# Optimization experiments

Hardware: AMD Instinct MI355X
Metric: run time of the kernel (lower is better)

Reference implementation:

```python
import jax, jax.numpy as jnp
import numpy as np

OUTDIM, INPUTDIM, DEGREE = 64, 512, 8


def setup_inputs() -> dict:
    key = jax.random.key(0)
    k1, k2 = jax.random.split(key)
    x = jax.random.normal(k1, (16, 4096, INPUTDIM), dtype=jnp.float32)
    # torch.randn(outdim, inputdim, degree) / (sqrt(inputdim)*sqrt(degree))
    coeffs = jax.random.normal(k2, (OUTDIM, INPUTDIM, DEGREE), dtype=jnp.float32)
    coeffs = coeffs / (np.sqrt(INPUTDIM) * np.sqrt(DEGREE))
    bias = jnp.zeros((1, OUTDIM), dtype=jnp.float32)
    return {"x": x, "coeffs": coeffs, "bias": bias}


def _legendre_basis(xn, degree):
    # Iterative (memoized) Legendre recurrence; xn in [-1, 1], shape [N, I].
    Ps = [jnp.ones_like(xn)]
    if degree > 1:
        Ps.append(xn)
    for n in range(2, degree):
        Ps.append(((2.0 * n - 1.0) * xn * Ps[-1] - (n - 1.0) * Ps[-2]) / n)
    return jnp.stack(Ps, axis=-1)  # [N, I, D]


def reference(x, coeffs, bias):
    outdim, inputdim, degree = coeffs.shape
    outshape = x.shape[:-1] + (outdim,)
    x2 = x.reshape(-1, inputdim)                      # [N, I]
    xmin, xmax = x2.min(), x2.max()                   # global min-max normalize
    xn = 2.0 * (x2 - xmin) / (xmax - xmin) - 1.0
    P = _legendre_basis(xn, degree)                   # [N, I, D]
    y = jnp.einsum("nid,oid->no", P, coeffs)          # contract input & degree
    y = y + bias                                      # [N, O]
    return y.reshape(outshape)
```

## Files before the change

### kernel.cpp

```cpp
#include <hip/hip_runtime.h>
#include <math.h>


typedef __bf16 bf16x8 __attribute__((ext_vector_type(8)));
typedef float f32x4 __attribute__((ext_vector_type(4)));

__global__ __launch_bounds__(256) void k_minmax_partial(
    const float4* __restrict__ x4, int n4, float* __restrict__ pmn, float* __restrict__ pmx)
{
  float mn = 3.4e38f, mx = -3.4e38f;
  int stride = gridDim.x * 256;
  for (int i = blockIdx.x * 256 + threadIdx.x; i < n4; i += stride) {
    float4 v = x4[i];
    mn = fminf(mn, fminf(fminf(v.x, v.y), fminf(v.z, v.w)));
    mx = fmaxf(mx, fmaxf(fmaxf(v.x, v.y), fmaxf(v.z, v.w)));
  }
  #pragma unroll
  for (int off = 32; off > 0; off >>= 1) {
    mn = fminf(mn, __shfl_down(mn, off));
    mx = fmaxf(mx, __shfl_down(mx, off));
  }
  __shared__ float smn[4], smx[4];
  int w = threadIdx.x >> 6;
  if ((threadIdx.x & 63) == 0) { smn[w] = mn; smx[w] = mx; }
  __syncthreads();
  if (threadIdx.x == 0) {
    pmn[blockIdx.x] = fminf(fminf(smn[0], smn[1]), fminf(smn[2], smn[3]));
    pmx[blockIdx.x] = fmaxf(fmaxf(smx[0], smx[1]), fmaxf(smx[2], smx[3]));
  }
}

__global__ __launch_bounds__(256) void k_prep_final(
    const float* __restrict__ coeffs, bf16x8* __restrict__ Bws,
    const float* __restrict__ pmn, const float* __restrict__ pmx, int nb,
    float* __restrict__ so)
{
  if (blockIdx.x < 128) {
    int t = blockIdx.x * 256 + threadIdx.x;
    int lane = t & 63;
    int tile = t >> 6;
    int ct = tile & 3;
    int kt = tile >> 2;
    int i = kt * 4 + (lane >> 4);
    int o = ct * 16 + (lane & 15);
    const float4* cp = (const float4*)(coeffs + ((size_t)o * 512 + i) * 8);
    float4 c0 = cp[0], c1 = cp[1];
    bf16x8 v;
    v[0] = (__bf16)(c0.x);
    v[1] = (__bf16)(c0.y);
    v[2] = (__bf16)(c0.z * 1.5f);
    v[3] = (__bf16)(c0.w * 2.5f);
    v[4] = (__bf16)(c1.x * 4.375f);
    v[5] = (__bf16)(c1.y * 7.875f);
    v[6] = (__bf16)(c1.z * 14.4375f);
    v[7] = (__bf16)(c1.w * 26.8125f);
    Bws[(size_t)(kt * 4 + ct) * 64 + lane] = v;
  } else {
    float mn = 3.4e38f, mx = -3.4e38f;
    for (int i = threadIdx.x; i < nb; i += 256) {
      mn = fminf(mn, pmn[i]);
      mx = fmaxf(mx, pmx[i]);
    }
    #pragma unroll
    for (int off = 32; off > 0; off >>= 1) {
      mn = fminf(mn, __shfl_down(mn, off));
      mx = fmaxf(mx, __shfl_down(mx, off));
    }
    __shared__ float smn[4], smx[4];
    int w = threadIdx.x >> 6;
    if ((threadIdx.x & 63) == 0) { smn[w] = mn; smx[w] = mx; }
    __syncthreads();
    if (threadIdx.x == 0) {
      mn = fminf(fminf(smn[0], smn[1]), fminf(smn[2], smn[3]));
      mx = fmaxf(fmaxf(smx[0], smx[1]), fmaxf(smx[2], smx[3]));
      float r = mx - mn;
      so[0] = 2.0f / r;
      so[1] = -2.0f * mn / r - 1.0f;
    }
  }
}

#define LSTW 20
__global__ __launch_bounds__(256, 3) void k_main(
    const float* __restrict__ x, const bf16x8* __restrict__ Bws,
    const float* __restrict__ bias, const float* __restrict__ so,
    float* __restrict__ y)
{
  __shared__ char smem[49152];

  const float s = so[0], off = so[1];
  const int t    = threadIdx.x;
  const int lane = t & 63;
  const int w    = t >> 6;
  const int m    = lane & 15;
  const int quad = lane >> 4;
  const size_t blockRow = (size_t)blockIdx.x * 64;

  float* xsw = (float*)(smem + w * (2 * 64 * LSTW * 4));
  const float* xg = x + (blockRow + lane) * 512 + w * 128;

  int rb[4];
  #pragma unroll
  for (int f = 0; f < 4; ++f) rb[f] = (f * 16 + m) * LSTW + quad;

  const bf16x8* Bp = Bws + (size_t)w * 32 * 256 + lane;

  f32x4 acc[4][4];
  #pragma unroll
  for (int f = 0; f < 4; ++f)
    #pragma unroll
    for (int ct = 0; ct < 4; ++ct) acc[f][ct] = (f32x4){0.f, 0.f, 0.f, 0.f};

  const float C2 = 0.33333334f, C3 = 0.26666668f, C4 = 0.25714287f;
  const float C5 = 0.25396827f, C6 = 0.25252524f, C7 = 0.25174826f;

  float4 st[4];
  #pragma unroll
  for (int p = 0; p < 4; ++p) st[p] = *(const float4*)(xg + p * 4);
  #pragma unroll
  for (int p = 0; p < 4; ++p) *(float4*)&xsw[lane * LSTW + p * 4] = st[p];

  bf16x8 Bq[4][4];
  #pragma unroll
  for (int ct = 0; ct < 4; ++ct) {
    Bq[0][ct] = Bp[ct * 64];
    Bq[1][ct] = Bp[256 + ct * 64];
  }

  for (int c = 0; c < 8; ++c) {
    float* xr = xsw + (c & 1) * (64 * LSTW);

    if (c < 7) {
      const float* gp = xg + (c + 1) * 16;
      #pragma unroll
      for (int p = 0; p < 4; ++p) st[p] = *(const float4*)(gp + p * 4);
    }

    float xv[2][4];
    #pragma unroll
    for (int f = 0; f < 4; ++f) xv[0][f] = xr[rb[f]];

    #pragma unroll
    for (int ktl = 0; ktl < 4; ++ktl) {
      const int l = c * 4 + ktl;

      {
        const int kp = (l + 2) & 31;
        const bf16x8* bpk = Bp + (size_t)kp * 256;
        #pragma unroll
        for (int ct = 0; ct < 4; ++ct) Bq[(ktl + 2) & 3][ct] = bpk[ct * 64];
      }
      if (ktl < 3) {
        #pragma unroll
        for (int f = 0; f < 4; ++f)
          xv[(ktl + 1) & 1][f] = xr[rb[f] + (ktl + 1) * 4];
      }

      bf16x8 a[4];
      #pragma unroll
      for (int f = 0; f < 4; ++f) {
        float xn = fmaf(xv[ktl & 1][f], s, off);
        float s2 = fmaf(xn, xn, -C2);
        float s3 = (s2 - C3) * xn;
        float s4 = fmaf(xn, s3, -(C4 * s2));
        float s5 = fmaf(xn, s4, -(C5 * s3));
        float s6 = fmaf(xn, s5, -(C6 * s4));
        float s7 = fmaf(xn, s6, -(C7 * s5));
        bf16x8 av;
        av[0] = (__bf16)1.0f; av[1] = (__bf16)xn; av[2] = (__bf16)s2; av[3] = (__bf16)s3;
        av[4] = (__bf16)s4;   av[5] = (__bf16)s5; av[6] = (__bf16)s6; av[7] = (__bf16)s7;
        a[f] = av;
      }

      #pragma unroll
      for (int f = 0; f < 4; ++f)
        #pragma unroll
        for (int ct = 0; ct < 4; ++ct)
          acc[f][ct] = __builtin_amdgcn_mfma_f32_16x16x32_bf16(a[f], Bq[ktl & 3][ct], acc[f][ct], 0, 0, 0);
    }

    if (c < 7) {
      float* xw = xsw + ((c + 1) & 1) * (64 * LSTW);
      #pragma unroll
      for (int p = 0; p < 4; ++p) *(float4*)&xw[lane * LSTW + p * 4] = st[p];
    }
  }

  __syncthreads();
  f32x4* red = (f32x4*)smem;
  if (w > 0) {
    #pragma unroll
    for (int f = 0; f < 4; ++f)
      #pragma unroll
      for (int ct = 0; ct < 4; ++ct)
        red[(size_t)(w - 1) * 1024 + (f * 4 + ct) * 64 + lane] = acc[f][ct];
  }
  __syncthreads();
  if (w == 0) {
    #pragma unroll
    for (int f = 0; f < 4; ++f)
      #pragma unroll
      for (int ct = 0; ct < 4; ++ct) {
        f32x4 v = acc[f][ct];
        v += red[(f * 4 + ct) * 64 + lane];
        v += red[1024 + (f * 4 + ct) * 64 + lane];
        v += red[2048 + (f * 4 + ct) * 64 + lane];
        acc[f][ct] = v;
      }
    float bv0 = bias[m], bv1 = bias[16 + m], bv2 = bias[32 + m], bv3 = bias[48 + m];
    #pragma unroll
    for (int f = 0; f < 4; ++f) {
      float* yp = y + (blockRow + f * 16 + quad * 4) * 64 + m;
      #pragma unroll
      for (int r = 0; r < 4; ++r) {
        float* ypr = yp + r * 64;
        ypr[0]  = acc[f][0][r] + bv0;
        ypr[16] = acc[f][1][r] + bv1;
        ypr[32] = acc[f][2][r] + bv2;
        ypr[48] = acc[f][3][r] + bv3;
      }
    }
  }
}

__global__ __launch_bounds__(256) void k_main_simple(
    const float* __restrict__ x, const float* __restrict__ coeffs,
    const float* __restrict__ bias, const float* __restrict__ so, float* __restrict__ y)
{
  const float s = so[0], off = so[1];
  const int lane = threadIdx.x & 63;
  const int w    = threadIdx.x >> 6;
  const int m    = lane & 15;
  const int quad = lane >> 4;
  const int rowA = blockIdx.x * 64 + w * 16 + m;
  const float* xp = x + (size_t)rowA * 512 + quad;

  f32x4 acc0 = {0.f,0.f,0.f,0.f}, acc1 = acc0, acc2 = acc0, acc3 = acc0;
  const float c3a = 5.f/3.f, c3b = 2.f/3.f, c6a = 11.f/6.f, c6b = 5.f/6.f, c7a = 13.f/7.f, c7b = 6.f/7.f;

  for (int kt = 0; kt < 128; ++kt) {
    float xv = xp[kt * 4];
    int i = kt * 4 + quad;
    bf16x8 b[4];
    #pragma unroll
    for (int ct = 0; ct < 4; ++ct) {
      const float* cp = coeffs + ((size_t)(ct * 16 + m) * 512 + i) * 8;
      #pragma unroll
      for (int j = 0; j < 8; ++j) b[ct][j] = (__bf16)cp[j];
    }
    float xn = fmaf(xv, s, off);
    float p2 = fmaf(1.5f * xn, xn, -0.5f);
    float p3 = fmaf(c3a * xn, p2, -(c3b * xn));
    float p4 = fmaf(1.75f * xn, p3, -(0.75f * p2));
    float p5 = fmaf(1.8f * xn, p4, -(0.8f * p3));
    float p6 = fmaf(c6a * xn, p5, -(c6b * p4));
    float p7 = fmaf(c7a * xn, p6, -(c7b * p5));
    bf16x8 a;
    a[0] = (__bf16)1.0f; a[1] = (__bf16)xn; a[2] = (__bf16)p2; a[3] = (__bf16)p3;
    a[4] = (__bf16)p4;   a[5] = (__bf16)p5; a[6] = (__bf16)p6; a[7] = (__bf16)p7;
    acc0 = __builtin_amdgcn_mfma_f32_16x16x32_bf16(a, b[0], acc0, 0, 0, 0);
    acc1 = __builtin_amdgcn_mfma_f32_16x16x32_bf16(a, b[1], acc1, 0, 0, 0);
    acc2 = __builtin_amdgcn_mfma_f32_16x16x32_bf16(a, b[2], acc2, 0, 0, 0);
    acc3 = __builtin_amdgcn_mfma_f32_16x16x32_bf16(a, b[3], acc3, 0, 0, 0);
  }
  float b0v = bias[m], b1v = bias[16+m], b2v = bias[32+m], b3v = bias[48+m];
  float* yp = y + ((size_t)(blockIdx.x * 64 + w * 16 + quad * 4)) * 64 + m;
  #pragma unroll
  for (int r = 0; r < 4; ++r) {
    yp[r*64+ 0] = acc0[r] + b0v;
    yp[r*64+16] = acc1[r] + b1v;
    yp[r*64+32] = acc2[r] + b2v;
    yp[r*64+48] = acc3[r] + b3v;
  }
}

extern "C" void kernel_launch(void* const* d_in, const int* in_sizes, int n_in,
                              void* d_out, int out_size, void* d_ws, size_t ws_size,
                              hipStream_t stream)
{
  const float* x      = (const float*)d_in[0];
  const float* coeffs = (const float*)d_in[1];
  const float* bias   = (const float*)d_in[2];
  float* y = (float*)d_out;

  long nx = (long)in_sizes[0];
  int  N  = (int)(nx / 512);
  int  n4 = (int)(nx / 4);

  float*  so  = (float*)d_ws;
  float*  pmn = (float*)d_ws + 16;
  float*  pmx = pmn + 4096;
  bf16x8* Bws = (bf16x8*)((char*)d_ws + 65536);

  const int MMB = 2048;
  k_minmax_partial<<<MMB, 256, 0, stream>>>((const float4*)x, n4, pmn, pmx);

  bool pre = ws_size >= (size_t)(65536 + 4096 * 64 * 2 + 4096);
  k_prep_final<<<129, 256, 0, stream>>>(coeffs, Bws, pmn, pmx, MMB, so);
  if (pre) {
    k_main<<<N / 64, 256, 0, stream>>>(x, Bws, bias, so, y);
  } else {
    k_main_simple<<<N / 64, 256, 0, stream>>>(x, coeffs, bias, so, y);
  }
}
```

Baseline: 252.3 us.

## Split K across blocks with atomic accumulation and LDS-staged coefficients

```diff
diff --git a/kernel.cpp b/kernel.cpp
--- a/kernel.cpp
+++ b/kernel.cpp
@@ -33,10 +33,13 @@
 __global__ __launch_bounds__(256) void k_prep_final(
     const float* __restrict__ coeffs, bf16x8* __restrict__ Bws,
     const float* __restrict__ pmn, const float* __restrict__ pmx, int nb,
-    float* __restrict__ so)
-{
-  if (blockIdx.x < 128) {
-    int t = blockIdx.x * 256 + threadIdx.x;
+    float* __restrict__ so, float* __restrict__ y, const float* __restrict__ bias,
+    int doB)
+{
+  int b = blockIdx.x;
+  if (b < 128) {
+    if (!doB) return;
+    int t = b * 256 + threadIdx.x;
     int lane = t & 63;
     int tile = t >> 6;
     int ct = tile & 3;
@@ -55,7 +58,7 @@
     v[6] = (__bf16)(c1.z * 14.4375f);
     v[7] = (__bf16)(c1.w * 26.8125f);
     Bws[(size_t)(kt * 4 + ct) * 64 + lane] = v;
-  } else {
+  } else if (b == 128) {
     float mn = 3.4e38f, mx = -3.4e38f;
     for (int i = threadIdx.x; i < nb; i += 256) {
       mn = fminf(mn, pmn[i]);
@@ -77,16 +80,23 @@
       so[0] = 2.0f / r;
       so[1] = -2.0f * mn / r - 1.0f;
     }
-  }
-}
-
-#define LSTW 20
-__global__ __launch_bounds__(256, 3) void k_main(
+  } else {
+    int base = (b - 129) * 1024;
+    const float4* b4 = (const float4*)bias;
+    float4* y4 = (float4*)y;
+    #pragma unroll
+    for (int r = 0; r < 4; ++r) {
+      int j = base + r * 256 + threadIdx.x;
+      y4[j] = b4[j & 15];
+    }
+  }
+}
+
+__global__ __launch_bounds__(256, 4) void k_main(
     const float* __restrict__ x, const bf16x8* __restrict__ Bws,
-    const float* __restrict__ bias, const float* __restrict__ so,
-    float* __restrict__ y)
-{
-  __shared__ char smem[49152];
+    const float* __restrict__ so, float* __restrict__ y)
+{
+  __shared__ __align__(16) float4 smem[2048];
 
   const float s = so[0], off = so[1];
   const int t    = threadIdx.x;
@@ -94,72 +104,65 @@
   const int w    = t >> 6;
   const int m    = lane & 15;
   const int quad = lane >> 4;
-  const size_t blockRow = (size_t)blockIdx.x * 64;
-
-  float* xsw = (float*)(smem + w * (2 * 64 * LSTW * 4));
-  const float* xg = x + (blockRow + lane) * 512 + w * 128;
-
-  int rb[4];
-  #pragma unroll
-  for (int f = 0; f < 4; ++f) rb[f] = (f * 16 + m) * LSTW + quad;
-
-  const bf16x8* Bp = Bws + (size_t)w * 32 * 256 + lane;
-
-  f32x4 acc[4][4];
-  #pragma unroll
-  for (int f = 0; f < 4; ++f)
+  const int bx   = blockIdx.x;
+  const int qK   = bx & 3;
+  const size_t rowbase = ((size_t)(bx >> 2)) * 128 + (size_t)w * 32;
+  const int kb0 = qK * 32;
+
+  const float* xq0 = x + (rowbase +      m) * 512 + (size_t)kb0 * 4 + quad;
+  const float* xq1 = x + (rowbase + 16 + m) * 512 + (size_t)kb0 * 4 + quad;
+
+  const float4* bsrc = (const float4*)((const char*)Bws + (size_t)kb0 * 4096);
+
+  f32x4 acc[2][4];
+  #pragma unroll
+  for (int f = 0; f < 2; ++f)
     #pragma unroll
     for (int ct = 0; ct < 4; ++ct) acc[f][ct] = (f32x4){0.f, 0.f, 0.f, 0.f};
 
   const float C2 = 0.33333334f, C3 = 0.26666668f, C4 = 0.25714287f;
   const float C5 = 0.25396827f, C6 = 0.25252524f, C7 = 0.25174826f;
 
-  float4 st[4];
-  #pragma unroll
-  for (int p = 0; p < 4; ++p) st[p] = *(const float4*)(xg + p * 4);
-  #pragma unroll
-  for (int p = 0; p < 4; ++p) *(float4*)&xsw[lane * LSTW + p * 4] = st[p];
-
-  bf16x8 Bq[4][4];
-  #pragma unroll
-  for (int ct = 0; ct < 4; ++ct) {
-    Bq[0][ct] = Bp[ct * 64];
-    Bq[1][ct] = Bp[256 + ct * 64];
-  }
-
-  for (int c = 0; c < 8; ++c) {
-    float* xr = xsw + (c & 1) * (64 * LSTW);
-
-    if (c < 7) {
-      const float* gp = xg + (c + 1) * 16;
-      #pragma unroll
-      for (int p = 0; p < 4; ++p) st[p] = *(const float4*)(gp + p * 4);
-    }
-
-    float xv[2][4];
-    #pragma unroll
-    for (int f = 0; f < 4; ++f) xv[0][f] = xr[rb[f]];
-
-    #pragma unroll
-    for (int ktl = 0; ktl < 4; ++ktl) {
-      const int l = c * 4 + ktl;
-
+  float xr[4][2];
+  xr[0][0] = xq0[0];  xr[0][1] = xq1[0];
+  xr[1][0] = xq0[4];  xr[1][1] = xq1[4];
+
+  const bf16x8* bw = (const bf16x8*)smem;
+
+  for (int wi = 0; wi < 4; ++wi) {
+    __syncthreads();
+    {
+      const float4* g = bsrc + (size_t)wi * 2048;
+      float4 a0 = g[t], a1 = g[t + 256], a2 = g[t + 512], a3 = g[t + 768];
+      smem[t] = a0; smem[t + 256] = a1; smem[t + 512] = a2; smem[t + 768] = a3;
+      float4 b0 = g[t + 1024], b1 = g[t + 1280], b2 = g[t + 1536], b3 = g[t + 1792];
+      smem[t + 1024] = b0; smem[t + 1280] = b1; smem[t + 1536] = b2; smem[t + 1792] = b3;
+    }
+    __syncthreads();
+
+    bf16x8 Bq[2][4];
+    #pragma unroll
+    for (int ct = 0; ct < 4; ++ct) Bq[0][ct] = bw[ct * 64 + lane];
+
+    #pragma unroll
+    for (int kl = 0; kl < 8; ++kl) {
+      const int l = wi * 8 + kl;
+
+      if (kl < 7) {
+        #pragma unroll
+        for (int ct = 0; ct < 4; ++ct)
+          Bq[(kl + 1) & 1][ct] = bw[((kl + 1) * 4 + ct) * 64 + lane];
+      }
       {
-        const int kp = (l + 2) & 31;
-        const bf16x8* bpk = Bp + (size_t)kp * 256;
-        #pragma unroll
-        for (int ct = 0; ct < 4; ++ct) Bq[(ktl + 2) & 3][ct] = bpk[ct * 64];
+        const int lp = (l + 2 < 32) ? (l + 2) : 31;
+        xr[(kl + 2) & 3][0] = xq0[lp * 4];
+        xr[(kl + 2) & 3][1] = xq1[lp * 4];
       }
-      if (ktl < 3) {
-        #pragma unroll
-        for (int f = 0; f < 4; ++f)
-          xv[(ktl + 1) & 1][f] = xr[rb[f] + (ktl + 1) * 4];
-      }
-
-      bf16x8 a[4];
-      #pragma unroll
-      for (int f = 0; f < 4; ++f) {
-        float xn = fmaf(xv[ktl & 1][f], s, off);
+
+      bf16x8 a[2];
+      #pragma unroll
+      for (int f = 0; f < 2; ++f) {
+        float xn = fmaf(xr[kl & 3][f], s, off);
         float s2 = fmaf(xn, xn, -C2);
         float s3 = (s2 - C3) * xn;
         float s4 = fmaf(xn, s3, -(C4 * s2));
@@ -173,53 +176,21 @@
       }
 
       #pragma unroll
-      for (int f = 0; f < 4; ++f)
+      for (int f = 0; f < 2; ++f)
         #pragma unroll
         for (int ct = 0; ct < 4; ++ct)
-          acc[f][ct] = __builtin_amdgcn_mfma_f32_16x16x32_bf16(a[f], Bq[ktl & 3][ct], acc[f][ct], 0, 0, 0);
-    }
-
-    if (c < 7) {
-      float* xw = xsw + ((c + 1) & 1) * (64 * LSTW);
-      #pragma unroll
-      for (int p = 0; p < 4; ++p) *(float4*)&xw[lane * LSTW + p * 4] = st[p];
-    }
-  }
-
-  __syncthreads();
-  f32x4* red = (f32x4*)smem;
-  if (w > 0) {
-    #pragma unroll
-    for (int f = 0; f < 4; ++f)
-      #pragma unroll
-      for (int ct = 0; ct < 4; ++ct)
-        red[(size_t)(w - 1) * 1024 + (f * 4 + ct) * 64 + lane] = acc[f][ct];
-  }
-  __syncthreads();
-  if (w == 0) {
-    #pragma unroll
-    for (int f = 0; f < 4; ++f)
-      #pragma unroll
-      for (int ct = 0; ct < 4; ++ct) {
-        f32x4 v = acc[f][ct];
-        v += red[(f * 4 + ct) * 64 + lane];
-        v += red[1024 + (f * 4 + ct) * 64 + lane];
-        v += red[2048 + (f * 4 + ct) * 64 + lane];
-        acc[f][ct] = v;
-      }
-    float bv0 = bias[m], bv1 = bias[16 + m], bv2 = bias[32 + m], bv3 = bias[48 + m];
-    #pragma unroll
-    for (int f = 0; f < 4; ++f) {
-      float* yp = y + (blockRow + f * 16 + quad * 4) * 64 + m;
-      #pragma unroll
-      for (int r = 0; r < 4; ++r) {
-        float* ypr = yp + r * 64;
-        ypr[0]  = acc[f][0][r] + bv0;
-        ypr[16] = acc[f][1][r] + bv1;
-        ypr[32] = acc[f][2][r] + bv2;
-        ypr[48] = acc[f][3][r] + bv3;
-      }
-    }
+          acc[f][ct] = __builtin_amdgcn_mfma_f32_16x16x32_bf16(a[f], Bq[kl & 1][ct], acc[f][ct], 0, 0, 0);
+    }
+  }
+
+  #pragma unroll
+  for (int f = 0; f < 2; ++f) {
+    float* yp = y + (rowbase + f * 16 + quad * 4) * 64 + m;
+    #pragma unroll
+    for (int ct = 0; ct < 4; ++ct)
+      #pragma unroll
+      for (int r = 0; r < 4; ++r)
+        atomicAdd(yp + r * 64 + ct * 16, acc[f][ct][r]);
   }
 }
 
@@ -292,13 +263,14 @@
   float*  pmx = pmn + 4096;
   bf16x8* Bws = (bf16x8*)((char*)d_ws + 65536);
 
-  const int MMB = 2048;
+  bool pre = ws_size >= (size_t)(65536 + 4096 * 64 * 2 + 4096);
+
+  const int MMB = 4096;
   k_minmax_partial<<<MMB, 256, 0, stream>>>((const float4*)x, n4, pmn, pmx);
-
-  bool pre = ws_size >= (size_t)(65536 + 4096 * 64 * 2 + 4096);
-  k_prep_final<<<129, 256, 0, stream>>>(coeffs, Bws, pmn, pmx, MMB, so);
+  k_prep_final<<<1153, 256, 0, stream>>>(coeffs, Bws, pmn, pmx, MMB, so, y, bias, pre ? 1 : 0);
+
   if (pre) {
-    k_main<<<N / 64, 256, 0, stream>>>(x, Bws, bias, so, y);
+    k_main<<<(N / 128) * 4, 256, 0, stream>>>(x, Bws, so, y);
   } else {
     k_main_simple<<<N / 64, 256, 0, stream>>>(x, coeffs, bias, so, y);
   }
```

After: 284.3 us. 12.7% more time.
